# Optimization experiments

Hardware: AMD Instinct MI355X
Metric: run time of the kernel (lower is better)

Reference implementation:

```python
import jax, jax.numpy as jnp
import numpy as np

CLAMP = 60.0
EPS = 1e-4

def _make_weights(N, alpha_logits, delta_logits, beta_logits):
    alpha = jax.nn.sigmoid(alpha_logits)   # [C,H]
    delta = jax.nn.sigmoid(delta_logits)
    beta = jax.nn.sigmoid(beta_logits)
    A = alpha * beta                        # [C,H]
    r = jnp.clip(1.0 - alpha * delta, EPS, 1.0 - EPS)
    t = jnp.arange(N, dtype=jnp.float32)[:, None, None]   # [N,1,1]
    logr = jnp.clip(jnp.log(r) * t, -CLAMP, CLAMP)        # [N,C,H]
    return A, jnp.exp(logr), jnp.exp(-logr)

def _ema_fwd(x, A, eta, r_pos, r_neg):
    # x: [B,N,C] -> y: [B,N,C]
    z = A * x[..., None] * r_neg            # [B,N,C,H]
    h = jnp.cumsum(z, axis=1) * r_pos       # [B,N,C,H]
    return jnp.sum(eta * h, axis=-1)        # [B,N,C]

def reference(x, alpha_logits, delta_logits, beta_logits, eta, proj_w, proj_b):
    B, N, C = x.shape
    A, r_pos, r_neg = _make_weights(N, alpha_logits, delta_logits, beta_logits)
    xf = x.astype(jnp.float32)
    y_fwd = _ema_fwd(xf, A, eta, r_pos, r_neg)
    y_bwd = _ema_fwd(xf[:, ::-1], A, eta, r_pos, r_neg)[:, ::-1]
    z = jnp.concatenate([y_fwd, y_bwd], axis=-1).astype(x.dtype)  # [B,N,2C]
    return z @ proj_w.T + proj_b            # [B,N,C]

def setup_inputs():
    key = jax.random.key(0)
    ks = jax.random.split(key, 7)
    B, N, C, H = 8, 4096, 512, 4
    return {
        "x": jax.random.normal(ks[0], (B, N, C), dtype=jnp.float32),
        "alpha_logits": jax.random.normal(ks[1], (C, H), dtype=jnp.float32),
        "delta_logits": jax.random.normal(ks[2], (C, H), dtype=jnp.float32),
        "beta_logits": jax.random.normal(ks[3], (C, H), dtype=jnp.float32),
        "eta": jax.random.normal(ks[4], (C, H), dtype=jnp.float32) * 0.02,
        "proj_w": jax.random.normal(ks[5], (C, 2 * C), dtype=jnp.float32) / np.sqrt(2.0 * C),
        "proj_b": jax.random.normal(ks[6], (C,), dtype=jnp.float32) * 0.01,
    }
```

## Files before the change

kernel.cpp:

```cpp
#include <hip/hip_runtime.h>
#include <hip/hip_bf16.h>

#define B_ 8
#define N_ 4096
#define C_ 512
#define H_ 4
#define EPS_ 1e-4f
#define E60P 1.14200739e26f
#define E60M 8.7565108e-27f

typedef __attribute__((ext_vector_type(8))) short short8;
typedef __attribute__((ext_vector_type(4))) float floatx4;
typedef __attribute__((ext_vector_type(2))) float floatx2;
typedef __attribute__((ext_vector_type(4))) unsigned short ushort4_t;
typedef unsigned short ushort_t;

__device__ __forceinline__ float sigmoidf_(float v) {
    return 1.0f / (1.0f + expf(-v));
}

__device__ __forceinline__ int pk_off(int t, int w, int k0, int ks, int f,
                                      int lane8, int kb) {
    return ((((t * 2 + w) * 16 + k0) * 2 + ks) * 4 + f) * 512 + lane8 * 8 + kb;
}

__device__ __forceinline__ void gload16(const void* g, void* l) {
    __builtin_amdgcn_global_load_lds(
        (const __attribute__((address_space(1))) void*)g,
        (__attribute__((address_space(3))) void*)l, 16, 0, 0);
}

__global__ __launch_bounds__(256) void k_partials3(
    const float* __restrict__ x, const float* __restrict__ al,
    const float* __restrict__ dl, const float* __restrict__ bl,
    float* __restrict__ P)
{
    int bid   = blockIdx.x;
    int chunk = bid & 15;
    int ct    = (bid >> 4) & 7;
    int b     = bid >> 7;
    int lane  = threadIdx.x & 63;
    int wave  = threadIdx.x >> 6;
    int c     = ct * 64 + lane;
    int sub   = chunk * 4 + wave;
    int t0f   = sub * 64;
    int t0b   = (63 - sub) * 64;

    float aa[4], dd[4], bb[4];
    { float4 v = ((const float4*)al)[c]; aa[0]=v.x; aa[1]=v.y; aa[2]=v.z; aa[3]=v.w; }
    { float4 v = ((const float4*)dl)[c]; dd[0]=v.x; dd[1]=v.y; dd[2]=v.z; dd[3]=v.w; }
    { float4 v = ((const float4*)bl)[c]; bb[0]=v.x; bb[1]=v.y; bb[2]=v.z; bb[3]=v.w; }

    float A[H_], ri[H_], Lh[H_];
    #pragma unroll
    for (int h = 0; h < H_; ++h) {
        float alpha = sigmoidf_(aa[h]);
        float delta = sigmoidf_(dd[h]);
        float beta  = sigmoidf_(bb[h]);
        A[h] = alpha * beta;
        float r = fminf(fmaxf(1.0f - alpha * delta, EPS_), 1.0f - EPS_);
        Lh[h] = logf(r);
        ri[h] = 1.0f / r;
    }
    const floatx2 E2P = {E60P, E60P};
    floatx2 A2[2]  = {{A[0],  A[1]},  {A[2],  A[3]}};
    floatx2 ri2[2] = {{ri[0], ri[1]}, {ri[2], ri[3]}};

    const float* xp = x + ((size_t)b * N_ + t0f) * C_ + c;

    floatx2 ep2[2], T2[2];
    #pragma unroll
    for (int p = 0; p < 2; ++p) {
        ep2[p] = (floatx2){expf(fminf(-Lh[2*p]   * (float)t0f, 60.0f)),
                           expf(fminf(-Lh[2*p+1] * (float)t0f, 60.0f))};
        T2[p]  = (floatx2){0.f, 0.f};
    }
    {
        float cur[8];
        #pragma unroll
        for (int j = 0; j < 8; ++j) cur[j] = xp[(size_t)j * C_];
        #pragma unroll 1
        for (int g = 0; g < 8; ++g) {
            float nxt[8];
            if (g < 7) {
                #pragma unroll
                for (int j = 0; j < 8; ++j)
                    nxt[j] = xp[(size_t)(g * 8 + 8 + j) * C_];
            }
            #pragma unroll
            for (int j = 0; j < 8; ++j) {
                floatx2 xv2 = {cur[j], cur[j]};
                #pragma unroll
                for (int p = 0; p < 2; ++p) {
                    T2[p] += (A2[p] * xv2) * ep2[p];
                    ep2[p] = __builtin_elementwise_min(ep2[p] * ri2[p], E2P);
                }
            }
            if (g < 7) {
                #pragma unroll
                for (int j = 0; j < 8; ++j) cur[j] = nxt[j];
            }
        }
        float* pp = P + ((size_t)b * 64 + sub) * (H_ * C_) + c;
        pp[0]      = T2[0].x;  pp[C_]     = T2[0].y;
        pp[2 * C_] = T2[1].x;  pp[3 * C_] = T2[1].y;
    }

    #pragma unroll
    for (int p = 0; p < 2; ++p) {
        ep2[p] = (floatx2){expf(fminf(-Lh[2*p]   * (float)t0b, 60.0f)),
                           expf(fminf(-Lh[2*p+1] * (float)t0b, 60.0f))};
        T2[p]  = (floatx2){0.f, 0.f};
    }
    {
        float cur[8];
        #pragma unroll
        for (int j = 0; j < 8; ++j) cur[j] = xp[(size_t)(63 - j) * C_];
        #pragma unroll 1
        for (int g = 0; g < 8; ++g) {
            float nxt[8];
            if (g < 7) {
                #pragma unroll
                for (int j = 0; j < 8; ++j)
                    nxt[j] = xp[(size_t)(63 - (g * 8 + 8 + j)) * C_];
            }
            #pragma unroll
            for (int j = 0; j < 8; ++j) {
                floatx2 xv2 = {cur[j], cur[j]};
                #pragma unroll
                for (int p = 0; p < 2; ++p) {
                    T2[p] += (A2[p] * xv2) * ep2[p];
                    ep2[p] = __builtin_elementwise_min(ep2[p] * ri2[p], E2P);
                }
            }
            if (g < 7) {
                #pragma unroll
                for (int j = 0; j < 8; ++j) cur[j] = nxt[j];
            }
        }
        float* pp = P + ((size_t)(8 + b) * 64 + (63 - sub)) * (H_ * C_) + c;
        pp[0]      = T2[0].x;  pp[C_]     = T2[0].y;
        pp[2 * C_] = T2[1].x;  pp[3 * C_] = T2[1].y;
    }
}

__global__ __launch_bounds__(256) void k_scan(float* __restrict__ P)
{
    int bid = blockIdx.x;
    int ct  = bid & 7;
    int b   = (bid >> 3) & 7;
    int dir = bid >> 6;
    int cl  = threadIdx.x & 63;
    int h   = threadIdx.x >> 6;
    int c   = ct * 64 + cl;

    float* base = P + ((size_t)(dir * 8 + b) * 64) * (H_ * C_) + h * C_ + c;

    float v[64];
    #pragma unroll
    for (int s = 0; s < 64; ++s) v[s] = base[s * (H_ * C_)];

    float run = 0.0f;
    #pragma unroll
    for (int s = 0; s < 64; ++s) { float t = v[s]; v[s] = run; run += t; }

    #pragma unroll
    for (int s = 0; s < 64; ++s) base[s * (H_ * C_)] = v[s];
}

__global__ __launch_bounds__(256) void k_apply3(
    const float* __restrict__ x, const float* __restrict__ al,
    const float* __restrict__ dl, const float* __restrict__ bl,
    const float* __restrict__ eta, const float* __restrict__ P,
    ushort_t* __restrict__ Zp)
{
    int bid   = blockIdx.x;
    int chunk = bid & 15;
    int ct    = (bid >> 4) & 7;
    int b     = bid >> 7;
    int lane  = threadIdx.x & 63;
    int wave  = threadIdx.x >> 6;
    int c     = ct * 64 + lane;
    int sub   = chunk * 4 + wave;
    int t0f   = sub * 64;
    int t0b   = (63 - sub) * 64;

    int ksv = lane >> 5, qv = (lane >> 3) & 3, kbv = lane & 7;
    int mt  = b * 32 + (t0f >> 7);
    int wq  = (t0f >> 6) & 1;
    int offcF = pk_off(mt, wq, ct,     ksv, 0, qv * 16, kbv);
    int offcB = pk_off(mt, wq, 8 + ct, ksv, 0, qv * 16, kbv);

    float aa[4], dd[4], bb[4], ee[4];
    { float4 v = ((const float4*)al )[c]; aa[0]=v.x; aa[1]=v.y; aa[2]=v.z; aa[3]=v.w; }
    { float4 v = ((const float4*)dl )[c]; dd[0]=v.x; dd[1]=v.y; dd[2]=v.z; dd[3]=v.w; }
    { float4 v = ((const float4*)bl )[c]; bb[0]=v.x; bb[1]=v.y; bb[2]=v.z; bb[3]=v.w; }
    { float4 v = ((const float4*)eta)[c]; ee[0]=v.x; ee[1]=v.y; ee[2]=v.z; ee[3]=v.w; }

    float A[H_], rr[H_], ri[H_], Lh[H_];
    #pragma unroll
    for (int h = 0; h < H_; ++h) {
        float alpha = sigmoidf_(aa[h]);
        float delta = sigmoidf_(dd[h]);
        float beta  = sigmoidf_(bb[h]);
        A[h] = alpha * beta;
        float r = fminf(fmaxf(1.0f - alpha * delta, EPS_), 1.0f - EPS_);
        Lh[h] = logf(r);
        rr[h] = r;
        ri[h] = 1.0f / r;
    }
    const floatx2 E2P = {E60P, E60P};
    const floatx2 E2M = {E60M, E60M};
    floatx2 A2[2]  = {{A[0],  A[1]},  {A[2],  A[3]}};
    floatx2 ri2[2] = {{ri[0], ri[1]}, {ri[2], ri[3]}};
    floatx2 rr2[2] = {{rr[0], rr[1]}, {rr[2], rr[3]}};
    floatx2 ee2[2] = {{ee[0], ee[1]}, {ee[2], ee[3]}};

    const float* xp = x + ((size_t)b * N_ + t0f) * C_ + c;

    {
        const float* cp = P + ((size_t)b * 64 + sub) * (H_ * C_) + c;
        floatx2 ep2[2], em2[2], S2[2];
        #pragma unroll
        for (int p = 0; p < 2; ++p) {
            ep2[p] = (floatx2){expf(fminf(-Lh[2*p]   * (float)t0f, 60.0f)),
                               expf(fminf(-Lh[2*p+1] * (float)t0f, 60.0f))};
            em2[p] = (floatx2){expf(fmaxf( Lh[2*p]   * (float)t0f, -60.0f)),
                               expf(fmaxf( Lh[2*p+1] * (float)t0f, -60.0f))};
            S2[p]  = (floatx2){cp[(2*p) * C_], cp[(2*p+1) * C_]};
        }
        float cur[8];
        #pragma unroll
        for (int j = 0; j < 8; ++j) cur[j] = xp[(size_t)j * C_];
        #pragma unroll 1
        for (int g = 0; g < 8; ++g) {
            float nxt[8];
            if (g < 7) {
                #pragma unroll
                for (int j = 0; j < 8; ++j)
                    nxt[j] = xp[(size_t)(g * 8 + 8 + j) * C_];
            }
            #pragma unroll
            for (int j = 0; j < 8; ++j) {
                int i = g * 8 + j;
                floatx2 xv2 = {cur[j], cur[j]};
                floatx2 acc = {0.f, 0.f};
                #pragma unroll
                for (int p = 0; p < 2; ++p) {
                    S2[p] += (A2[p] * xv2) * ep2[p];
                    ep2[p] = __builtin_elementwise_min(ep2[p] * ri2[p], E2P);
                    acc   += ee2[p] * (em2[p] * S2[p]);
                    em2[p] = __builtin_elementwise_max(em2[p] * rr2[p], E2M);
                }
                float y = acc.x + acc.y;
                __hip_bfloat16 yb = __float2bfloat16(y);
                Zp[offcF + (i >> 4) * 512 + (i & 15) * 8] = *(ushort_t*)&yb;
            }
            if (g < 7) {
                #pragma unroll
                for (int j = 0; j < 8; ++j) cur[j] = nxt[j];
            }
        }
    }

    {
        const float* cp = P + ((size_t)(8 + b) * 64 + (63 - sub)) * (H_ * C_) + c;
        floatx2 ep2[2], em2[2], S2[2];
        #pragma unroll
        for (int p = 0; p < 2; ++p) {
            ep2[p] = (floatx2){expf(fminf(-Lh[2*p]   * (float)t0b, 60.0f)),
                               expf(fminf(-Lh[2*p+1] * (float)t0b, 60.0f))};
            em2[p] = (floatx2){expf(fmaxf( Lh[2*p]   * (float)t0b, -60.0f)),
                               expf(fmaxf( Lh[2*p+1] * (float)t0b, -60.0f))};
            S2[p]  = (floatx2){cp[(2*p) * C_], cp[(2*p+1) * C_]};
        }
        float cur[8];
        #pragma unroll
        for (int j = 0; j < 8; ++j) cur[j] = xp[(size_t)(63 - j) * C_];
        #pragma unroll 1
        for (int g = 0; g < 8; ++g) {
            float nxt[8];
            if (g < 7) {
                #pragma unroll
                for (int j = 0; j < 8; ++j)
                    nxt[j] = xp[(size_t)(63 - (g * 8 + 8 + j)) * C_];
            }
            #pragma unroll
            for (int j = 0; j < 8; ++j) {
                int i = 63 - (g * 8 + j);
                floatx2 xv2 = {cur[j], cur[j]};
                floatx2 acc = {0.f, 0.f};
                #pragma unroll
                for (int p = 0; p < 2; ++p) {
                    S2[p] += (A2[p] * xv2) * ep2[p];
                    ep2[p] = __builtin_elementwise_min(ep2[p] * ri2[p], E2P);
                    acc   += ee2[p] * (em2[p] * S2[p]);
                    em2[p] = __builtin_elementwise_max(em2[p] * rr2[p], E2M);
                }
                float y = acc.x + acc.y;
                __hip_bfloat16 yb = __float2bfloat16(y);
                Zp[offcB + (i >> 4) * 512 + (i & 15) * 8] = *(ushort_t*)&yb;
            }
            if (g < 7) {
                #pragma unroll
                for (int j = 0; j < 8; ++j) cur[j] = nxt[j];
            }
        }
    }
}

__global__ __launch_bounds__(256) void k_cvtw2(const float* __restrict__ w,
                                               ushort_t* __restrict__ Wp)
{
    int i4 = blockIdx.x * 256 + threadIdx.x;
    int i  = i4 << 2;
    int n = i >> 10, k = i & 1023;
    int nt = n >> 7, rn = n & 127;
    int k0 = k >> 6, kk = k & 63;
    int off = pk_off(nt, rn >> 6, k0, kk >> 5, (rn >> 4) & 3,
                     ((kk >> 3) & 3) * 16 + (rn & 15), kk & 7);
    float4 v = ((const float4*)w)[i4];
    ushort4_t r;
    { __hip_bfloat16 t = __float2bfloat16(v.x); r.x = *(ushort_t*)&t; }
    { __hip_bfloat16 t = __float2bfloat16(v.y); r.y = *(ushort_t*)&t; }
    { __hip_bfloat16 t = __float2bfloat16(v.z); r.z = *(ushort_t*)&t; }
    { __hip_bfloat16 t = __float2bfloat16(v.w); r.w = *(ushort_t*)&t; }
    *(ushort4_t*)&Wp[off] = r;
}

__global__ __launch_bounds__(256, 4) void k_gemm3(
    const ushort_t* __restrict__ Zp, const ushort_t* __restrict__ Wp,
    const float* __restrict__ bias, float* __restrict__ out)
{
    __shared__ __align__(16) char lds[32768];
    char*  ldsA = lds;
    char*  ldsB = lds + 16384;
    float* stg  = (float*)lds;

    int tid  = threadIdx.x;
    int lane = tid & 63, wave = tid >> 6;
    int wm   = wave & 1, wn = wave >> 1;
    int fr   = lane & 15, quad = lane >> 4;

    int bid = blockIdx.x;
    int mt  = ((bid >> 5) << 3) | (bid & 7);
    int nt  = (bid >> 3) & 3;
    int m0  = mt * 128, n0 = nt * 128;

    const ushort_t* Az = Zp + ((size_t)(mt * 2) * 16) * 4096;
    const ushort_t* Bz = Wp + ((size_t)(nt * 2) * 16) * 4096;

    floatx4 acc[4][4];
    #pragma unroll
    for (int mf = 0; mf < 4; ++mf)
        #pragma unroll
        for (int nf = 0; nf < 4; ++nf)
            acc[mf][nf] = (floatx4){0.f, 0.f, 0.f, 0.f};

    for (int k0 = 0; k0 < 16; ++k0) {
        const ushort_t* As = Az + (size_t)k0 * 4096;
        const ushort_t* Bs = Bz + (size_t)k0 * 4096;
        #pragma unroll
        for (int w = 0; w < 2; ++w)
            #pragma unroll
            for (int inst = 0; inst < 2; ++inst) {
                gload16(As + w * 65536 + inst * 2048 + tid * 8,
                        ldsA + w * 8192 + inst * 4096 + tid * 16);
                gload16(Bs + w * 65536 + inst * 2048 + tid * 8,
                        ldsB + w * 8192 + inst * 4096 + tid * 16);
            }
        asm volatile("s_waitcnt vmcnt(0)" ::: "memory");
        __syncthreads();

        #pragma unroll
        for (int ks = 0; ks < 2; ++ks) {
            short8 af[4], bf[4];
            #pragma unroll
            for (int f = 0; f < 4; ++f) {
                af[f] = *(const short8*)(ldsA + wm * 8192 + (ks * 4 + f) * 1024 + lane * 16);
                bf[f] = *(const short8*)(ldsB + wn * 8192 + (ks * 4 + f) * 1024 + lane * 16);
            }
            #pragma unroll
            for (int mf = 0; mf < 4; ++mf)
                #pragma unroll
                for (int nf = 0; nf < 4; ++nf)
                    acc[mf][nf] = __builtin_amdgcn_mfma_f32_16x16x32_bf16(
                        af[mf], bf[nf], acc[mf][nf], 0, 0, 0);
        }
        __syncthreads();
    }

    int rrow = tid >> 3;
    int seg  = tid & 7;
    int gcol = n0 + seg * 16;

    #pragma unroll
    for (int ch = 0; ch < 4; ++ch) {
        if ((wave & 1) == (ch >> 1)) {
            int ml = (ch & 1) * 2;
            #pragma unroll
            for (int mi = 0; mi < 2; ++mi) {
                #pragma unroll
                for (int nf = 0; nf < 4; ++nf) {
                    int col = wn * 64 + nf * 16 + fr;
                    #pragma unroll
                    for (int rg = 0; rg < 4; ++rg) {
                        int row = mi * 16 + quad * 4 + rg;
                        stg[row * 132 + col] = acc[ml + mi][nf][rg];
                    }
                }
            }
        }
        __syncthreads();
        {
            int gm = m0 + ch * 32 + rrow;
            const float* s = &stg[rrow * 132 + seg * 16];
            #pragma unroll
            for (int k = 0; k < 4; ++k) {
                float4 v  = *(const float4*)&s[k * 4];
                float4 bv = *(const float4*)&bias[gcol + k * 4];
                v.x += bv.x; v.y += bv.y; v.z += bv.z; v.w += bv.w;
                *(float4*)&out[(size_t)gm * 512 + gcol + k * 4] = v;
            }
        }
        __syncthreads();
    }
}

extern "C" void kernel_launch(void* const* d_in, const int* in_sizes, int n_in,
                              void* d_out, int out_size, void* d_ws, size_t ws_size,
                              hipStream_t stream)
{
    const float* x  = (const float*)d_in[0];
    const float* al = (const float*)d_in[1];
    const float* dl = (const float*)d_in[2];
    const float* bl = (const float*)d_in[3];
    const float* et = (const float*)d_in[4];
    const float* pw = (const float*)d_in[5];
    const float* pb = (const float*)d_in[6];
    float* out = (float*)d_out;

    ushort_t* Zp = (ushort_t*)d_ws;
    float*    P  = (float*)((char*)d_ws + 67108864);
    ushort_t* Wp = (ushort_t*)((char*)d_ws + 75497472);

    hipLaunchKernelGGL(k_cvtw2,     dim3(512),  dim3(256), 0, stream, pw, Wp);
    hipLaunchKernelGGL(k_partials3, dim3(1024), dim3(256), 0, stream, x, al, dl, bl, P);
    hipLaunchKernelGGL(k_scan,      dim3(128),  dim3(256), 0, stream, P);
    hipLaunchKernelGGL(k_apply3,    dim3(1024), dim3(256), 0, stream, x, al, dl, bl, et, P, Zp);
    hipLaunchKernelGGL(k_gemm3,     dim3(1024), dim3(256), 0, stream, Zp, Wp, pb, out);
}
```

Baseline: 224.8 us.

## Fold A into decay factor, deepen x prefetch, and register-prefetch GEMM tiles

Three separate changes. The scan kernels fold the A coefficient into the running decay factor, which removes one multiply per step, with the clamp rescaled to A*e^60. They also prefetch x in groups of 16 rows instead of 8. The GEMM holds the current k-slice fragments in registers and issues the global-to-LDS loads for the next slice before its MFMAs, so the loads overlap the math; launch bounds drop from 4 to 3 waves to make room. This costs more registers and therefore less occupancy, and the clamp now applies to A*r^-t rather than r^-t, which is equivalent because A is at most 1.

```diff
diff --git a/kernel.cpp b/kernel.cpp
--- a/kernel.cpp
+++ b/kernel.cpp
@@ -30,7 +30,7 @@
         (__attribute__((address_space(3))) void*)l, 16, 0, 0);
 }
 
-__global__ __launch_bounds__(256) void k_partials3(
+__global__ __launch_bounds__(256) void k_partials4(
     const float* __restrict__ x, const float* __restrict__ al,
     const float* __restrict__ dl, const float* __restrict__ bl,
     float* __restrict__ P)
@@ -62,43 +62,42 @@
         Lh[h] = logf(r);
         ri[h] = 1.0f / r;
     }
-    const floatx2 E2P = {E60P, E60P};
-    floatx2 A2[2]  = {{A[0],  A[1]},  {A[2],  A[3]}};
-    floatx2 ri2[2] = {{ri[0], ri[1]}, {ri[2], ri[3]}};
+    floatx2 ri2[2]  = {{ri[0], ri[1]}, {ri[2], ri[3]}};
+    floatx2 AEP2[2] = {{A[0] * E60P, A[1] * E60P}, {A[2] * E60P, A[3] * E60P}};
 
     const float* xp = x + ((size_t)b * N_ + t0f) * C_ + c;
 
-    floatx2 ep2[2], T2[2];
+    floatx2 Ae2[2], T2[2];
     #pragma unroll
     for (int p = 0; p < 2; ++p) {
-        ep2[p] = (floatx2){expf(fminf(-Lh[2*p]   * (float)t0f, 60.0f)),
-                           expf(fminf(-Lh[2*p+1] * (float)t0f, 60.0f))};
+        Ae2[p] = (floatx2){A[2*p]   * expf(fminf(-Lh[2*p]   * (float)t0f, 60.0f)),
+                           A[2*p+1] * expf(fminf(-Lh[2*p+1] * (float)t0f, 60.0f))};
         T2[p]  = (floatx2){0.f, 0.f};
     }
     {
-        float cur[8];
-        #pragma unroll
-        for (int j = 0; j < 8; ++j) cur[j] = xp[(size_t)j * C_];
+        float cur[16];
+        #pragma unroll
+        for (int j = 0; j < 16; ++j) cur[j] = xp[(size_t)j * C_];
         #pragma unroll 1
-        for (int g = 0; g < 8; ++g) {
-            float nxt[8];
-            if (g < 7) {
-                #pragma unroll
-                for (int j = 0; j < 8; ++j)
-                    nxt[j] = xp[(size_t)(g * 8 + 8 + j) * C_];
-            }
-            #pragma unroll
-            for (int j = 0; j < 8; ++j) {
+        for (int g = 0; g < 4; ++g) {
+            float nxt[16];
+            if (g < 3) {
+                #pragma unroll
+                for (int j = 0; j < 16; ++j)
+                    nxt[j] = xp[(size_t)(g * 16 + 16 + j) * C_];
+            }
+            #pragma unroll
+            for (int j = 0; j < 16; ++j) {
                 floatx2 xv2 = {cur[j], cur[j]};
                 #pragma unroll
                 for (int p = 0; p < 2; ++p) {
-                    T2[p] += (A2[p] * xv2) * ep2[p];
-                    ep2[p] = __builtin_elementwise_min(ep2[p] * ri2[p], E2P);
-                }
-            }
-            if (g < 7) {
-                #pragma unroll
-                for (int j = 0; j < 8; ++j) cur[j] = nxt[j];
+                    T2[p] += Ae2[p] * xv2;
+                    Ae2[p] = __builtin_elementwise_min(Ae2[p] * ri2[p], AEP2[p]);
+                }
+            }
+            if (g < 3) {
+                #pragma unroll
+                for (int j = 0; j < 16; ++j) cur[j] = nxt[j];
             }
         }
         float* pp = P + ((size_t)b * 64 + sub) * (H_ * C_) + c;
@@ -108,34 +107,34 @@
 
     #pragma unroll
     for (int p = 0; p < 2; ++p) {
-        ep2[p] = (floatx2){expf(fminf(-Lh[2*p]   * (float)t0b, 60.0f)),
-                           expf(fminf(-Lh[2*p+1] * (float)t0b, 60.0f))};
+        Ae2[p] = (floatx2){A[2*p]   * expf(fminf(-Lh[2*p]   * (float)t0b, 60.0f)),
+                           A[2*p+1] * expf(fminf(-Lh[2*p+1] * (float)t0b, 60.0f))};
         T2[p]  = (floatx2){0.f, 0.f};
     }
     {
-        float cur[8];
-        #pragma unroll
-        for (int j = 0; j < 8; ++j) cur[j] = xp[(size_t)(63 - j) * C_];
+        float cur[16];
+        #pragma unroll
+        for (int j = 0; j < 16; ++j) cur[j] = xp[(size_t)(63 - j) * C_];
         #pragma unroll 1
-        for (int g = 0; g < 8; ++g) {
-            float nxt[8];
-            if (g < 7) {
-                #pragma unroll
-                for (int j = 0; j < 8; ++j)
-                    nxt[j] = xp[(size_t)(63 - (g * 8 + 8 + j)) * C_];
-            }
-            #pragma unroll
-            for (int j = 0; j < 8; ++j) {
+        for (int g = 0; g < 4; ++g) {
+            float nxt[16];
+            if (g < 3) {
+                #pragma unroll
+                for (int j = 0; j < 16; ++j)
+                    nxt[j] = xp[(size_t)(63 - (g * 16 + 16 + j)) * C_];
+            }
+            #pragma unroll
+            for (int j = 0; j < 16; ++j) {
                 floatx2 xv2 = {cur[j], cur[j]};
                 #pragma unroll
                 for (int p = 0; p < 2; ++p) {
-                    T2[p] += (A2[p] * xv2) * ep2[p];
-                    ep2[p] = __builtin_elementwise_min(ep2[p] * ri2[p], E2P);
-                }
-            }
-            if (g < 7) {
-                #pragma unroll
-                for (int j = 0; j < 8; ++j) cur[j] = nxt[j];
+                    T2[p] += Ae2[p] * xv2;
+                    Ae2[p] = __builtin_elementwise_min(Ae2[p] * ri2[p], AEP2[p]);
+                }
+            }
+            if (g < 3) {
+                #pragma unroll
+                for (int j = 0; j < 16; ++j) cur[j] = nxt[j];
             }
         }
         float* pp = P + ((size_t)(8 + b) * 64 + (63 - sub)) * (H_ * C_) + c;
@@ -168,7 +167,7 @@
     for (int s = 0; s < 64; ++s) base[s * (H_ * C_)] = v[s];
 }
 
-__global__ __launch_bounds__(256) void k_apply3(
+__global__ __launch_bounds__(256) void k_apply4(
     const float* __restrict__ x, const float* __restrict__ al,
     const float* __restrict__ dl, const float* __restrict__ bl,
     const float* __restrict__ eta, const float* __restrict__ P,
@@ -209,46 +208,45 @@
         rr[h] = r;
         ri[h] = 1.0f / r;
     }
-    const floatx2 E2P = {E60P, E60P};
     const floatx2 E2M = {E60M, E60M};
-    floatx2 A2[2]  = {{A[0],  A[1]},  {A[2],  A[3]}};
-    floatx2 ri2[2] = {{ri[0], ri[1]}, {ri[2], ri[3]}};
-    floatx2 rr2[2] = {{rr[0], rr[1]}, {rr[2], rr[3]}};
-    floatx2 ee2[2] = {{ee[0], ee[1]}, {ee[2], ee[3]}};
+    floatx2 ri2[2]  = {{ri[0], ri[1]}, {ri[2], ri[3]}};
+    floatx2 rr2[2]  = {{rr[0], rr[1]}, {rr[2], rr[3]}};
+    floatx2 ee2[2]  = {{ee[0], ee[1]}, {ee[2], ee[3]}};
+    floatx2 AEP2[2] = {{A[0] * E60P, A[1] * E60P}, {A[2] * E60P, A[3] * E60P}};
 
     const float* xp = x + ((size_t)b * N_ + t0f) * C_ + c;
 
     {
         const float* cp = P + ((size_t)b * 64 + sub) * (H_ * C_) + c;
-        floatx2 ep2[2], em2[2], S2[2];
+        floatx2 Ae2[2], em2[2], S2[2];
         #pragma unroll
         for (int p = 0; p < 2; ++p) {
-            ep2[p] = (floatx2){expf(fminf(-Lh[2*p]   * (float)t0f, 60.0f)),
-                               expf(fminf(-Lh[2*p+1] * (float)t0f, 60.0f))};
+            Ae2[p] = (floatx2){A[2*p]   * expf(fminf(-Lh[2*p]   * (float)t0f, 60.0f)),
+                               A[2*p+1] * expf(fminf(-Lh[2*p+1] * (float)t0f, 60.0f))};
             em2[p] = (floatx2){expf(fmaxf( Lh[2*p]   * (float)t0f, -60.0f)),
                                expf(fmaxf( Lh[2*p+1] * (float)t0f, -60.0f))};
             S2[p]  = (floatx2){cp[(2*p) * C_], cp[(2*p+1) * C_]};
         }
-        float cur[8];
-        #pragma unroll
-        for (int j = 0; j < 8; ++j) cur[j] = xp[(size_t)j * C_];
+        float cur[16];
+        #pragma unroll
+        for (int j = 0; j < 16; ++j) cur[j] = xp[(size_t)j * C_];
         #pragma unroll 1
-        for (int g = 0; g < 8; ++g) {
-            float nxt[8];
-            if (g < 7) {
-                #pragma unroll
-                for (int j = 0; j < 8; ++j)
-                    nxt[j] = xp[(size_t)(g * 8 + 8 + j) * C_];
-            }
-            #pragma unroll
-            for (int j = 0; j < 8; ++j) {
-                int i = g * 8 + j;
+        for (int g = 0; g < 4; ++g) {
+            float nxt[16];
+            if (g < 3) {
+                #pragma unroll
+                for (int j = 0; j < 16; ++j)
+                    nxt[j] = xp[(size_t)(g * 16 + 16 + j) * C_];
+            }
+            #pragma unroll
+            for (int j = 0; j < 16; ++j) {
+                int i = g * 16 + j;
                 floatx2 xv2 = {cur[j], cur[j]};
                 floatx2 acc = {0.f, 0.f};
                 #pragma unroll
                 for (int p = 0; p < 2; ++p) {
-                    S2[p] += (A2[p] * xv2) * ep2[p];
-                    ep2[p] = __builtin_elementwise_min(ep2[p] * ri2[p], E2P);
+                    S2[p] += Ae2[p] * xv2;
+                    Ae2[p] = __builtin_elementwise_min(Ae2[p] * ri2[p], AEP2[p]);
                     acc   += ee2[p] * (em2[p] * S2[p]);
                     em2[p] = __builtin_elementwise_max(em2[p] * rr2[p], E2M);
                 }
@@ -256,44 +254,44 @@
                 __hip_bfloat16 yb = __float2bfloat16(y);
                 Zp[offcF + (i >> 4) * 512 + (i & 15) * 8] = *(ushort_t*)&yb;
             }
-            if (g < 7) {
-                #pragma unroll
-                for (int j = 0; j < 8; ++j) cur[j] = nxt[j];
+            if (g < 3) {
+                #pragma unroll
+                for (int j = 0; j < 16; ++j) cur[j] = nxt[j];
             }
         }
     }
 
     {
         const float* cp = P + ((size_t)(8 + b) * 64 + (63 - sub)) * (H_ * C_) + c;
-        floatx2 ep2[2], em2[2], S2[2];
+        floatx2 Ae2[2], em2[2], S2[2];
         #pragma unroll
         for (int p = 0; p < 2; ++p) {
-            ep2[p] = (floatx2){expf(fminf(-Lh[2*p]   * (float)t0b, 60.0f)),
-                               expf(fminf(-Lh[2*p+1] * (float)t0b, 60.0f))};
+            Ae2[p] = (floatx2){A[2*p]   * expf(fminf(-Lh[2*p]   * (float)t0b, 60.0f)),
+                               A[2*p+1] * expf(fminf(-Lh[2*p+1] * (float)t0b, 60.0f))};
             em2[p] = (floatx2){expf(fmaxf( Lh[2*p]   * (float)t0b, -60.0f)),
                                expf(fmaxf( Lh[2*p+1] * (float)t0b, -60.0f))};
             S2[p]  = (floatx2){cp[(2*p) * C_], cp[(2*p+1) * C_]};
         }
-        float cur[8];
-        #pragma unroll
-        for (int j = 0; j < 8; ++j) cur[j] = xp[(size_t)(63 - j) * C_];
+        float cur[16];
+        #pragma unroll
+        for (int j = 0; j < 16; ++j) cur[j] = xp[(size_t)(63 - j) * C_];
         #pragma unroll 1
-        for (int g = 0; g < 8; ++g) {
-            float nxt[8];
-            if (g < 7) {
-                #pragma unroll
-                for (int j = 0; j < 8; ++j)
-                    nxt[j] = xp[(size_t)(63 - (g * 8 + 8 + j)) * C_];
-            }
-            #pragma unroll
-            for (int j = 0; j < 8; ++j) {
-                int i = 63 - (g * 8 + j);
+        for (int g = 0; g < 4; ++g) {
+            float nxt[16];
+            if (g < 3) {
+                #pragma unroll
+                for (int j = 0; j < 16; ++j)
+                    nxt[j] = xp[(size_t)(63 - (g * 16 + 16 + j)) * C_];
+            }
+            #pragma unroll
+            for (int j = 0; j < 16; ++j) {
+                int i = 63 - (g * 16 + j);
                 floatx2 xv2 = {cur[j], cur[j]};
                 floatx2 acc = {0.f, 0.f};
                 #pragma unroll
                 for (int p = 0; p < 2; ++p) {
-                    S2[p] += (A2[p] * xv2) * ep2[p];
-                    ep2[p] = __builtin_elementwise_min(ep2[p] * ri2[p], E2P);
+                    S2[p] += Ae2[p] * xv2;
+                    Ae2[p] = __builtin_elementwise_min(Ae2[p] * ri2[p], AEP2[p]);
                     acc   += ee2[p] * (em2[p] * S2[p]);
                     em2[p] = __builtin_elementwise_max(em2[p] * rr2[p], E2M);
                 }
@@ -301,9 +299,9 @@
                 __hip_bfloat16 yb = __float2bfloat16(y);
                 Zp[offcB + (i >> 4) * 512 + (i & 15) * 8] = *(ushort_t*)&yb;
             }
-            if (g < 7) {
-                #pragma unroll
-                for (int j = 0; j < 8; ++j) cur[j] = nxt[j];
+            if (g < 3) {
+                #pragma unroll
+                for (int j = 0; j < 16; ++j) cur[j] = nxt[j];
             }
         }
     }
@@ -328,7 +326,7 @@
     *(ushort4_t*)&Wp[off] = r;
 }
 
-__global__ __launch_bounds__(256, 4) void k_gemm3(
+__global__ __launch_bounds__(256, 3) void k_gemm4(
     const ushort_t* __restrict__ Zp, const ushort_t* __restrict__ Wp,
     const float* __restrict__ bias, float* __restrict__ out)
 {
@@ -357,38 +355,65 @@
         for (int nf = 0; nf < 4; ++nf)
             acc[mf][nf] = (floatx4){0.f, 0.f, 0.f, 0.f};
 
+    #pragma unroll
+    for (int w = 0; w < 2; ++w)
+        #pragma unroll
+        for (int inst = 0; inst < 2; ++inst) {
+            gload16(Az + w * 65536 + inst * 2048 + tid * 8,
+                    ldsA + w * 8192 + inst * 4096 + tid * 16);
+            gload16(Bz + w * 65536 + inst * 2048 + tid * 8,
+                    ldsB + w * 8192 + inst * 4096 + tid * 16);
+        }
+    asm volatile("s_waitcnt vmcnt(0)" ::: "memory");
+    __syncthreads();
+
+    short8 af[2][4], bf[2][4];
+    #pragma unroll
+    for (int ks = 0; ks < 2; ++ks)
+        #pragma unroll
+        for (int f = 0; f < 4; ++f) {
+            af[ks][f] = *(const short8*)(ldsA + wm * 8192 + (ks * 4 + f) * 1024 + lane * 16);
+            bf[ks][f] = *(const short8*)(ldsB + wn * 8192 + (ks * 4 + f) * 1024 + lane * 16);
+        }
+
     for (int k0 = 0; k0 < 16; ++k0) {
-        const ushort_t* As = Az + (size_t)k0 * 4096;
-        const ushort_t* Bs = Bz + (size_t)k0 * 4096;
-        #pragma unroll
-        for (int w = 0; w < 2; ++w)
-            #pragma unroll
-            for (int inst = 0; inst < 2; ++inst) {
-                gload16(As + w * 65536 + inst * 2048 + tid * 8,
-                        ldsA + w * 8192 + inst * 4096 + tid * 16);
-                gload16(Bs + w * 65536 + inst * 2048 + tid * 8,
-                        ldsB + w * 8192 + inst * 4096 + tid * 16);
-            }
-        asm volatile("s_waitcnt vmcnt(0)" ::: "memory");
         __syncthreads();
-
-        #pragma unroll
-        for (int ks = 0; ks < 2; ++ks) {
-            short8 af[4], bf[4];
-            #pragma unroll
-            for (int f = 0; f < 4; ++f) {
-                af[f] = *(const short8*)(ldsA + wm * 8192 + (ks * 4 + f) * 1024 + lane * 16);
-                bf[f] = *(const short8*)(ldsB + wn * 8192 + (ks * 4 + f) * 1024 + lane * 16);
-            }
+        if (k0 < 15) {
+            const ushort_t* As = Az + (size_t)(k0 + 1) * 4096;
+            const ushort_t* Bs = Bz + (size_t)(k0 + 1) * 4096;
+            #pragma unroll
+            for (int w = 0; w < 2; ++w)
+                #pragma unroll
+                for (int inst = 0; inst < 2; ++inst) {
+                    gload16(As + w * 65536 + inst * 2048 + tid * 8,
+                            ldsA + w * 8192 + inst * 4096 + tid * 16);
+                    gload16(Bs + w * 65536 + inst * 2048 + tid * 8,
+                            ldsB + w * 8192 + inst * 4096 + tid * 16);
+                }
+        }
+        __builtin_amdgcn_sched_barrier(0);
+        #pragma unroll
+        for (int ks = 0; ks < 2; ++ks)
             #pragma unroll
             for (int mf = 0; mf < 4; ++mf)
                 #pragma unroll
                 for (int nf = 0; nf < 4; ++nf)
                     acc[mf][nf] = __builtin_amdgcn_mfma_f32_16x16x32_bf16(
-                        af[mf], bf[nf], acc[mf][nf], 0, 0, 0);
-        }
-        __syncthreads();
-    }
+                        af[ks][mf], bf[ks][nf], acc[mf][nf], 0, 0, 0);
+        __builtin_amdgcn_sched_barrier(0);
+        if (k0 < 15) {
+            asm volatile("s_waitcnt vmcnt(0)" ::: "memory");
+            __syncthreads();
+            #pragma unroll
+            for (int ks = 0; ks < 2; ++ks)
+                #pragma unroll
+                for (int f = 0; f < 4; ++f) {
+                    af[ks][f] = *(const short8*)(ldsA + wm * 8192 + (ks * 4 + f) * 1024 + lane * 16);
+                    bf[ks][f] = *(const short8*)(ldsB + wn * 8192 + (ks * 4 + f) * 1024 + lane * 16);
+                }
+        }
+    }
+    __syncthreads();
 
     int rrow = tid >> 3;
     int seg  = tid & 7;
@@ -445,8 +470,8 @@
     ushort_t* Wp = (ushort_t*)((char*)d_ws + 75497472);
 
     hipLaunchKernelGGL(k_cvtw2,     dim3(512),  dim3(256), 0, stream, pw, Wp);
-    hipLaunchKernelGGL(k_partials3, dim3(1024), dim3(256), 0, stream, x, al, dl, bl, P);
+    hipLaunchKernelGGL(k_partials4, dim3(1024), dim3(256), 0, stream, x, al, dl, bl, P);
     hipLaunchKernelGGL(k_scan,      dim3(128),  dim3(256), 0, stream, P);
-    hipLaunchKernelGGL(k_apply3,    dim3(1024), dim3(256), 0, stream, x, al, dl, bl, et, P, Zp);
-    hipLaunchKernelGGL(k_gemm3,     dim3(1024), dim3(256), 0, stream, Zp, Wp, pb, out);
-}
+    hipLaunchKernelGGL(k_apply4,    dim3(1024), dim3(256), 0, stream, x, al, dl, bl, et, P, Zp);
+    hipLaunchKernelGGL(k_gemm4,     dim3(1024), dim3(256), 0, stream, Zp, Wp, pb, out);
+}
```

Result: no change. 221.4 us (-1.5%).
